# Optimization experiments

Measured on AMD Instinct MI355X. Metric: run time of the kernel, lower is better.

The kernel has to match this reference:

```python
import jax, jax.numpy as jnp
import numpy as np
import math

EMB_DIM = 1024
NUM_HEADS = 16
D_H = EMB_DIM // NUM_HEADS
B, S = 2, 2048


def setup_inputs() -> dict:
    key = jax.random.key(0)
    ks = jax.random.split(key, 6)
    limit = math.sqrt(6.0 / (EMB_DIM + D_H))  # xavier_uniform per head
    x = jax.random.normal(ks[0], (B, S, EMB_DIM), dtype=jnp.float32)
    Wq = jax.random.uniform(ks[1], (NUM_HEADS, EMB_DIM, D_H), jnp.float32, -limit, limit)
    Wk = jax.random.uniform(ks[2], (NUM_HEADS, EMB_DIM, D_H), jnp.float32, -limit, limit)
    Wv = jax.random.uniform(ks[3], (NUM_HEADS, EMB_DIM, D_H), jnp.float32, -limit, limit)
    bq = jnp.zeros((NUM_HEADS, D_H), jnp.float32)
    bk = jnp.zeros((NUM_HEADS, D_H), jnp.float32)
    bv = jnp.zeros((NUM_HEADS, D_H), jnp.float32)
    limo = math.sqrt(6.0 / (EMB_DIM + EMB_DIM))
    W_O = jax.random.uniform(ks[4], (EMB_DIM, EMB_DIM), jnp.float32, -limo, limo)
    causal_mask = jnp.tril(jnp.ones((S, S), jnp.float32))
    padding_mask = jnp.zeros((B, S), jnp.bool_)  # all-False: nothing padded
    return {"x": x, "Wq": Wq, "bq": bq, "Wk": Wk, "bk": bk, "Wv": Wv,
            "bv": bv, "W_O": W_O, "causal_mask": causal_mask,
            "padding_mask": padding_mask}


def reference(x, Wq, bq, Wk, bk, Wv, bv, W_O, causal_mask, padding_mask):
    # Per-head projections, vectorized over heads: [B,S,E] x [H,E,D] -> [B,H,S,D]
    Q = jnp.einsum('bse,hed->bhsd', x, Wq) + bq[None, :, None, :]
    K = jnp.einsum('bse,hed->bhsd', x, Wk) + bk[None, :, None, :]
    V = jnp.einsum('bse,hed->bhsd', x, Wv) + bv[None, :, None, :]
    scores = jnp.einsum('bhsd,bhtd->bhst', Q, K) / math.sqrt(D_H)
    neg_inf = jnp.float32(-jnp.inf)
    scores = jnp.where(causal_mask[None, None, :, :] == 0, neg_inf, scores)
    scores = jnp.where(padding_mask[:, None, None, :], neg_inf, scores)
    attn = jax.nn.softmax(scores, axis=-1)
    out = jnp.einsum('bhst,bhtd->bhsd', attn, V)  # [B,H,S,D]
    # concat heads in order (dim=-1) -> [B,S,H*D]
    x_concat = out.transpose(0, 2, 1, 3).reshape(B, S, EMB_DIM)
    return x_concat @ W_O
```

## Files before the change

kernel.cpp:

```cpp
#include <hip/hip_runtime.h>
#include <hip/hip_bf16.h>


typedef __hip_bfloat16 bf16;
typedef __attribute__((ext_vector_type(8))) short bfrag;
typedef __attribute__((ext_vector_type(4))) float f32x4;
typedef __attribute__((ext_vector_type(16))) float f32x16;
typedef __attribute__((ext_vector_type(4))) short short4v;

#define MFMA16(a, b, c) __builtin_amdgcn_mfma_f32_16x16x32_bf16(a, b, c, 0, 0, 0)
#define MFMA32(a, b, c) __builtin_amdgcn_mfma_f32_32x32x16_bf16(a, b, c, 0, 0, 0)

__device__ __forceinline__ unsigned pk2(float a, float b) {
  union { __hip_bfloat162 h; unsigned u; } w;
  w.h = __float22bfloat162_rn(make_float2(a, b));
  return w.u;
}

__device__ __forceinline__ void gload16(const bf16* g, bf16* l) {
  __builtin_amdgcn_global_load_lds(
      (const __attribute__((address_space(1))) void*)(g),
      (__attribute__((address_space(3))) void*)(l), 16, 0, 0);
}

__global__ __launch_bounds__(256) void prep_all(const float* __restrict__ x,
                                                const float* __restrict__ Wq,
                                                const float* __restrict__ Wk,
                                                const float* __restrict__ Wv,
                                                const float* __restrict__ Wo,
                                                bf16* __restrict__ xb,
                                                bf16* __restrict__ WqkvT,
                                                bf16* __restrict__ WoT) {
  __shared__ bf16 tile[64][80];
  int id = blockIdx.x;
  int t = threadIdx.x;
  if (id < 2048) {
    int i = id * 2048 + t * 8;
    float4 a = *(const float4*)(x + i);
    float4 b = *(const float4*)(x + i + 4);
    union { bf16 h[8]; bfrag v; } tmp;
    tmp.h[0] = __float2bfloat16(a.x); tmp.h[1] = __float2bfloat16(a.y);
    tmp.h[2] = __float2bfloat16(a.z); tmp.h[3] = __float2bfloat16(a.w);
    tmp.h[4] = __float2bfloat16(b.x); tmp.h[5] = __float2bfloat16(b.y);
    tmp.h[6] = __float2bfloat16(b.z); tmp.h[7] = __float2bfloat16(b.w);
    *(bfrag*)(xb + i) = tmp.v;
    return;
  }
  int wid = id - 2048;
  const float* src;
  bf16* dst;
  int srcld, dstld, r0, c0;
  if (wid < 768) {
    int w = wid >> 8, h = (wid >> 4) & 15;
    r0 = (wid & 15) * 64; c0 = 0;
    src = ((w == 0) ? Wq : (w == 1) ? Wk : Wv) + (long)h * 1024 * 64;
    dst = WqkvT + ((long)w * 1024 + h * 64) * 1024;
    srcld = 64; dstld = 1024;
  } else {
    int j = wid - 768;
    c0 = (j & 15) * 64; r0 = (j >> 4) * 64;
    src = Wo; dst = WoT;
    srcld = 1024; dstld = 1024;
  }
  int lr = t >> 3, lc = (t & 7) << 3;
#pragma unroll
  for (int p = 0; p < 2; ++p) {
    int r = lr + p * 32;
    const float* s = src + (long)(r0 + r) * srcld + c0 + lc;
    union { bf16 h8[8]; bfrag v; } tmp;
#pragma unroll
    for (int j = 0; j < 8; ++j) tmp.h8[j] = __float2bfloat16(s[j]);
    *(bfrag*)(&tile[r][lc]) = tmp.v;
  }
  __syncthreads();
#pragma unroll
  for (int p = 0; p < 2; ++p) {
    int c = lr + p * 32;
    union { bf16 h8[8]; bfrag v; } tmp;
#pragma unroll
    for (int j = 0; j < 8; ++j) tmp.h8[j] = tile[lc + j][c];
    *(bfrag*)(dst + (long)(c0 + c) * dstld + r0 + lc) = tmp.v;
  }
}

__global__ __launch_bounds__(256) void gemm_qkv128(const bf16* __restrict__ xb,
                                                   const bf16* __restrict__ WT,
                                                   const float* __restrict__ bq,
                                                   const float* __restrict__ bk,
                                                   const float* __restrict__ bv,
                                                   bf16* __restrict__ Q,
                                                   bf16* __restrict__ K_,
                                                   bf16* __restrict__ Vt) {
  const int K = 1024;
  __shared__ bf16 As[2][128 * 32];
  __shared__ bf16 Bs[2][128 * 32];
  int id = blockIdx.x;
  int xcd = id & 7, sw = id >> 3;
  int m0 = ((xcd << 2) | (sw & 3)) * 128;
  int n0 = (sw >> 2) * 128;
  int t = threadIdx.x, wave = t >> 6, lane = t & 63, quad = lane >> 4, col = lane & 15;
  int wr = (wave >> 1) * 64, wc = (wave & 1) * 64;
  f32x4 acc[4][4] = {};

  int schunk = (lane & 3) ^ ((lane >> 2) & 3);
  const bf16* Asrc = xb + (long)(m0 + wave * 32 + (lane >> 2)) * K + schunk * 8;
  const bf16* Bsrc = WT + (long)(n0 + wave * 32 + (lane >> 2)) * K + schunk * 8;
  int l0 = (wave * 32) * 32;
  int rdoff = ((quad ^ (col & 3)) << 3);

#define QKV_STAGE(bi, koff)                                    \
  {                                                            \
    gload16(Asrc + (koff), &As[bi][l0]);                       \
    gload16(Asrc + (koff) + 16 * K, &As[bi][l0 + 16 * 32]);    \
    gload16(Bsrc + (koff), &Bs[bi][l0]);                       \
    gload16(Bsrc + (koff) + 16 * K, &Bs[bi][l0 + 16 * 32]);    \
  }

  QKV_STAGE(0, 0);
  __syncthreads();
  for (int k0 = 0; k0 < K; k0 += 32) {
    int cur = (k0 >> 5) & 1;
    if (k0 + 32 < K) QKV_STAGE(cur ^ 1, k0 + 32);
    bfrag ra[4], rb[4];
#pragma unroll
    for (int i = 0; i < 4; ++i)
      ra[i] = *(const bfrag*)(&As[cur][(wr + 16 * i + col) * 32 + rdoff]);
#pragma unroll
    for (int c = 0; c < 4; ++c)
      rb[c] = *(const bfrag*)(&Bs[cur][(wc + 16 * c + col) * 32 + rdoff]);
#pragma unroll
    for (int c = 0; c < 4; ++c)
#pragma unroll
      for (int i = 0; i < 4; ++i) acc[c][i] = MFMA16(ra[i], rb[c], acc[c][i]);
    __syncthreads();
  }
#undef QKV_STAGE

  int sel = n0 >> 10;
  const float* bias = (sel == 0) ? bq : (sel == 1) ? bk : bv;
  float qs = (sel == 0) ? 0.18033688f : 1.0f;
#pragma unroll
  for (int c = 0; c < 4; ++c) {
    int nn = (n0 + wc + 16 * c + col) & 1023;
    float bvv = bias[nn];
    int h = nn >> 6, d = nn & 63;
#pragma unroll
    for (int i = 0; i < 4; ++i) {
      int mb = m0 + wr + 16 * i + quad * 4;
      int b = mb >> 11, s0 = mb & 2047;
      if (sel < 2) {
        bf16* dst = (sel == 0) ? Q : K_;
        long base = ((long)((b << 4) + h) * 2048 + s0) * 64 + d;
#pragma unroll
        for (int r = 0; r < 4; ++r)
          dst[base + (long)r * 64] = __float2bfloat16((acc[c][i][r] + bvv) * qs);
      } else {
        union { bf16 h4[4]; short4v v; } pk;
#pragma unroll
        for (int r = 0; r < 4; ++r) pk.h4[r] = __float2bfloat16(acc[c][i][r] + bvv);
        *(short4v*)(Vt + (long)(((b << 4) + h) * 64 + d) * 2048 + s0) = pk.v;
      }
    }
  }
}

__global__ __launch_bounds__(256) void gemm_out(const bf16* __restrict__ O,
                                                const bf16* __restrict__ Bt,
                                                float* __restrict__ Cf) {
  const int K = 1024;
  __shared__ bf16 As[2][128 * 32];
  __shared__ bf16 Bs[2][64 * 32];
  int id = blockIdx.x;
  int xcd = id & 7, sw = id >> 3;
  int m0 = ((xcd << 2) | (sw & 3)) * 128;
  int n0 = (sw >> 2) * 64;
  int t = threadIdx.x;
  int wave = t >> 6, lane = t & 63, quad = lane >> 4, col = lane & 15;
  int wr = (wave >> 1) * 64, wc = (wave & 1) * 32;
  f32x4 acc[2][4] = {};

  int schunk = (lane & 3) ^ ((lane >> 2) & 3);
  int arow = m0 + wave * 32 + (lane >> 2);
  int ob = arow >> 11, os = arow & 2047;
  const bf16* Asrc = O + (long)ob * 2097152 + (long)os * 64 + schunk * 8;
  const bf16* Bsrc = Bt + (long)(n0 + wave * 16 + (lane >> 2)) * K + schunk * 8;
  int la0 = (wave * 32) * 32;
  int lb0 = (wave * 16) * 32;
  int rdoff = ((quad ^ (col & 3)) << 3);

#define OUT_STAGE(bi, k0n)                                            \
  {                                                                   \
    long ka = ((long)((k0n) >> 6)) * 131072 + ((k0n) & 32);           \
    gload16(Asrc + ka, &As[bi][la0]);                                 \
    gload16(Asrc + ka + 16 * 64, &As[bi][la0 + 16 * 32]);             \
    gload16(Bsrc + (k0n), &Bs[bi][lb0]);                              \
  }

  OUT_STAGE(0, 0);
  __syncthreads();
  for (int k0 = 0; k0 < K; k0 += 32) {
    int cur = (k0 >> 5) & 1;
    if (k0 + 32 < K) OUT_STAGE(cur ^ 1, k0 + 32);
    bfrag ra[4], rb[2];
#pragma unroll
    for (int i = 0; i < 4; ++i)
      ra[i] = *(const bfrag*)(&As[cur][(wr + 16 * i + col) * 32 + rdoff]);
#pragma unroll
    for (int c = 0; c < 2; ++c)
      rb[c] = *(const bfrag*)(&Bs[cur][(wc + 16 * c + col) * 32 + rdoff]);
#pragma unroll
    for (int c = 0; c < 2; ++c)
#pragma unroll
      for (int i = 0; i < 4; ++i) acc[c][i] = MFMA16(ra[i], rb[c], acc[c][i]);
    __syncthreads();
  }
#undef OUT_STAGE

#pragma unroll
  for (int c = 0; c < 2; ++c) {
    int n = n0 + wc + 16 * c + col;
#pragma unroll
    for (int i = 0; i < 4; ++i)
#pragma unroll
      for (int r = 0; r < 4; ++r) {
        int m = m0 + wr + 16 * i + quad * 4 + r;
        Cf[(long)m * 1024 + n] = acc[c][i][r];
      }
  }
}

__global__ __launch_bounds__(256) void attn_kernel(const bf16* __restrict__ Q,
                                                   const bf16* __restrict__ K_,
                                                   const bf16* __restrict__ Vt,
                                                   bf16* __restrict__ O) {
  int id = blockIdx.x;
  int xcd = id & 7, jj = id >> 3;
  int qt = 31 - (jj >> 2);
  int bh = ((jj & 3) << 3) | xcd;

  __shared__ bf16 Ks[128][72];
  __shared__ bf16 Vs[64][136];

  int t = threadIdx.x, wave = t >> 6, lane = t & 63;
  int qh = wave >> 1, jh = wave & 1, hi = lane >> 5, l5 = lane & 31;

  int krow = t >> 3, kg = (t & 7) * 8;
  int vrow = t >> 4, vg = (t & 15) * 8;
  const bf16* KuBase = K_ + (long)bh * 2048 * 64;
  const bf16* VuBase = Vt + (long)bh * 64 * 2048;
  int kL = krow * 64 + kg;
  int vL = vrow * 2048 + vg;

  int q0 = qt * 64;
  int nj = (qt >> 1) + 1;
  int qi = q0 + 32 * qh + l5;

  bfrag qa[4];
  const bf16* qp = Q + ((long)bh * 2048 + q0 + 32 * qh + l5) * 64 + hi * 8;
#pragma unroll
  for (int kd = 0; kd < 4; ++kd) qa[kd] = *(const bfrag*)(qp + kd * 16);

  f32x16 o0, o1;
  float lsum = 0.f;
#pragma unroll
  for (int r = 0; r < 16; ++r) { o0[r] = 0.f; o1[r] = 0.f; }

  bfrag kreg[4], vreg[4];
#pragma unroll
  for (int i = 0; i < 4; ++i) {
    kreg[i] = *(const bfrag*)(KuBase + kL + i * 2048);
    vreg[i] = *(const bfrag*)(VuBase + vL + i * 32768);
  }

  for (int jt = 0; jt < nj; ++jt) {
    int j0 = jt * 128;
    __syncthreads();
#pragma unroll
    for (int i = 0; i < 4; ++i) {
      *(bfrag*)(&Ks[krow + 32 * i][kg]) = kreg[i];
      *(bfrag*)(&Vs[vrow + 16 * i][vg]) = vreg[i];
    }
    int jn = (jt + 1 < nj) ? j0 + 128 : j0;
    const bf16* kp = KuBase + (long)jn * 64;
    const bf16* vp = VuBase + jn;
#pragma unroll
    for (int i = 0; i < 4; ++i) {
      kreg[i] = *(const bfrag*)(kp + kL + i * 2048);
      vreg[i] = *(const bfrag*)(vp + vL + i * 32768);
    }
    __syncthreads();

    bool lastT = (jt == nj - 1);
    if (lastT && jh == 1 && ((qt & 1) == 0)) continue;

    f32x16 s0, s1;
#pragma unroll
    for (int r = 0; r < 16; ++r) { s0[r] = 0.f; s1[r] = 0.f; }
    __builtin_amdgcn_s_setprio(1);
#pragma unroll
    for (int kd = 0; kd < 4; ++kd) {
      bfrag ka0 = *(const bfrag*)(&Ks[jh * 64 + l5][kd * 16 + hi * 8]);
      bfrag ka1 = *(const bfrag*)(&Ks[jh * 64 + 32 + l5][kd * 16 + hi * 8]);
      s0 = MFMA32(ka0, qa[kd], s0);
      s1 = MFMA32(ka1, qa[kd], s1);
    }
    __builtin_amdgcn_s_setprio(0);

    unsigned g[2][4][2];
#pragma unroll
    for (int jb = 0; jb < 2; ++jb) {
      float pv[16];
      float ls = 0.f;
#pragma unroll
      for (int r = 0; r < 16; ++r) {
        int jl = (r & 3) + 8 * (r >> 2) + 4 * hi;
        int j = j0 + jh * 64 + jb * 32 + jl;
        float sv = jb ? s1[r] : s0[r];
        float p = __builtin_amdgcn_exp2f(sv);
        if (lastT) p = (j <= qi) ? p : 0.f;
        ls += p;
        pv[r] = p;
      }
      lsum += ls;
#pragma unroll
      for (int gg = 0; gg < 4; ++gg) {
        g[jb][gg][0] = pk2(pv[4 * gg], pv[4 * gg + 1]);
        g[jb][gg][1] = pk2(pv[4 * gg + 2], pv[4 * gg + 3]);
      }
    }

    __builtin_amdgcn_s_setprio(1);
#pragma unroll
    for (int jb = 0; jb < 2; ++jb) {
#pragma unroll
      for (int c = 0; c < 2; ++c) {
        unsigned a0 = g[jb][2 * c][0], a1 = g[jb][2 * c][1];
        unsigned b0 = g[jb][2 * c + 1][0], b1 = g[jb][2 * c + 1][1];
        asm("v_permlane32_swap_b32 %0, %1" : "+v"(a0), "+v"(b0));
        asm("v_permlane32_swap_b32 %0, %1" : "+v"(a1), "+v"(b1));
        union { unsigned u[4]; bfrag f; } pf;
        pf.u[0] = a0;
        pf.u[1] = a1;
        pf.u[2] = b0;
        pf.u[3] = b1;
        int kk = jh * 64 + jb * 32 + c * 16 + hi * 8;
        bfrag av0 = *(const bfrag*)(&Vs[l5][kk]);
        bfrag av1 = *(const bfrag*)(&Vs[32 + l5][kk]);
        o0 = MFMA32(av0, pf.f, o0);
        o1 = MFMA32(av1, pf.f, o1);
      }
    }
    __builtin_amdgcn_s_setprio(0);
  }

  lsum += __shfl_xor(lsum, 32, 64);

  __syncthreads();
  float* Osc = (float*)&Ks[0][0];
  float* Lsc = (float*)&Vs[0][0];
  bf16* Of = (bf16*)((char*)&Vs[0][0] + 512);
  int q = 32 * qh + l5;
  if (jh == 1) {
#pragma unroll
    for (int r = 0; r < 16; ++r) {
      int d = (r & 3) + 8 * (r >> 2) + 4 * hi;
      Osc[q * 68 + d] = o0[r];
      Osc[q * 68 + 32 + d] = o1[r];
    }
    if (hi == 0) Lsc[q] = lsum;
  }
  __syncthreads();
  if (jh == 0) {
    float inv = 1.f / (lsum + Lsc[q]);
#pragma unroll
    for (int r = 0; r < 16; ++r) {
      int d = (r & 3) + 8 * (r >> 2) + 4 * hi;
      Of[q * 72 + d] = __float2bfloat16((o0[r] + Osc[q * 68 + d]) * inv);
      Of[q * 72 + 32 + d] = __float2bfloat16((o1[r] + Osc[q * 68 + 32 + d]) * inv);
    }
  }
  __syncthreads();
  int row = t >> 2, off = (t & 3) * 16;
  bf16* po = O + ((long)bh * 2048 + q0 + row) * 64 + off;
  *(bfrag*)(po) = *(const bfrag*)(&Of[row * 72 + off]);
  *(bfrag*)(po + 8) = *(const bfrag*)(&Of[row * 72 + off + 8]);
}

extern "C" void kernel_launch(void* const* d_in, const int* in_sizes, int n_in,
                              void* d_out, int out_size, void* d_ws, size_t ws_size,
                              hipStream_t stream) {
  const float* x  = (const float*)d_in[0];
  const float* Wq = (const float*)d_in[1];
  const float* bq = (const float*)d_in[2];
  const float* Wk = (const float*)d_in[3];
  const float* bk = (const float*)d_in[4];
  const float* Wv = (const float*)d_in[5];
  const float* bv = (const float*)d_in[6];
  const float* Wo = (const float*)d_in[7];
  float* out = (float*)d_out;

  bf16* ws = (bf16*)d_ws;
  const long MB1 = 1 << 20;
  bf16* WqkvT = ws + 0 * MB1;
  bf16* WoT   = ws + 3 * MB1;
  bf16* Q     = ws + 4 * MB1;
  bf16* K_    = ws + 8 * MB1;
  bf16* Vt    = ws + 12 * MB1;
  bf16* O     = ws + 16 * MB1;
  bf16* xb    = ws + 20 * MB1;

  prep_all<<<3072, 256, 0, stream>>>(x, Wq, Wk, Wv, Wo, xb, WqkvT, WoT);
  gemm_qkv128<<<768, 256, 0, stream>>>(xb, WqkvT, bq, bk, bv, Q, K_, Vt);
  attn_kernel<<<1024, 256, 0, stream>>>(Q, K_, Vt, O);
  gemm_out<<<512, 256, 0, stream>>>(O, WoT, out);
}
```

Baseline: 194.8 us.

## Rewrite QKV GEMM as 256x256 tile, 8-wave kernel with phased prefetch pipeline

Replaces the 128x128 QKV projection GEMM with a 256x256-tile kernel using 512 threads, 128 KB of dynamic LDS with 64-wide K chunks, and an 8-phase software pipeline. Each phase interleaves LDS fragment reads, async global-to-LDS loads for later stages, raw barriers, and MFMA bursts under raised wave priority. The larger tile raises data reuse per byte loaded and the pipelining hides load latency. The cost is a grid of only 192 blocks and higher register and LDS pressure per block, which may hurt occupancy.

New measurement: 192.1 us. Within noise of the previous version (-1.4%).

```diff
diff --git a/kernel.cpp b/kernel.cpp
--- a/kernel.cpp
+++ b/kernel.cpp
@@ -21,6 +21,12 @@
   __builtin_amdgcn_global_load_lds(
       (const __attribute__((address_space(1))) void*)(g),
       (__attribute__((address_space(3))) void*)(l), 16, 0, 0);
+}
+
+__device__ __forceinline__ void barrier_raw() {
+  asm volatile("" ::: "memory");
+  __builtin_amdgcn_s_barrier();
+  asm volatile("" ::: "memory");
 }
 
 __global__ __launch_bounds__(256) void prep_all(const float* __restrict__ x,
@@ -83,82 +89,113 @@
   }
 }
 
-__global__ __launch_bounds__(256) void gemm_qkv128(const bf16* __restrict__ xb,
-                                                   const bf16* __restrict__ WT,
-                                                   const float* __restrict__ bq,
-                                                   const float* __restrict__ bk,
-                                                   const float* __restrict__ bv,
-                                                   bf16* __restrict__ Q,
-                                                   bf16* __restrict__ K_,
-                                                   bf16* __restrict__ Vt) {
-  const int K = 1024;
-  __shared__ bf16 As[2][128 * 32];
-  __shared__ bf16 Bs[2][128 * 32];
+__global__ __launch_bounds__(512, 2) void gemm_qkv128(const bf16* __restrict__ xb,
+                                                      const bf16* __restrict__ WT,
+                                                      const float* __restrict__ bq,
+                                                      const float* __restrict__ bk,
+                                                      const float* __restrict__ bv,
+                                                      bf16* __restrict__ Q,
+                                                      bf16* __restrict__ K_,
+                                                      bf16* __restrict__ Vt) {
+  extern __shared__ bf16 lds[];
   int id = blockIdx.x;
-  int xcd = id & 7, sw = id >> 3;
-  int m0 = ((xcd << 2) | (sw & 3)) * 128;
-  int n0 = (sw >> 2) * 128;
-  int t = threadIdx.x, wave = t >> 6, lane = t & 63, quad = lane >> 4, col = lane & 15;
-  int wr = (wave >> 1) * 64, wc = (wave & 1) * 64;
-  f32x4 acc[4][4] = {};
-
-  int schunk = (lane & 3) ^ ((lane >> 2) & 3);
-  const bf16* Asrc = xb + (long)(m0 + wave * 32 + (lane >> 2)) * K + schunk * 8;
-  const bf16* Bsrc = WT + (long)(n0 + wave * 32 + (lane >> 2)) * K + schunk * 8;
-  int l0 = (wave * 32) * 32;
-  int rdoff = ((quad ^ (col & 3)) << 3);
-
-#define QKV_STAGE(bi, koff)                                    \
-  {                                                            \
-    gload16(Asrc + (koff), &As[bi][l0]);                       \
-    gload16(Asrc + (koff) + 16 * K, &As[bi][l0 + 16 * 32]);    \
-    gload16(Bsrc + (koff), &Bs[bi][l0]);                       \
-    gload16(Bsrc + (koff) + 16 * K, &Bs[bi][l0 + 16 * 32]);    \
-  }
-
-  QKV_STAGE(0, 0);
-  __syncthreads();
-  for (int k0 = 0; k0 < K; k0 += 32) {
-    int cur = (k0 >> 5) & 1;
-    if (k0 + 32 < K) QKV_STAGE(cur ^ 1, k0 + 32);
-    bfrag ra[4], rb[4];
-#pragma unroll
-    for (int i = 0; i < 4; ++i)
-      ra[i] = *(const bfrag*)(&As[cur][(wr + 16 * i + col) * 32 + rdoff]);
-#pragma unroll
-    for (int c = 0; c < 4; ++c)
-      rb[c] = *(const bfrag*)(&Bs[cur][(wc + 16 * c + col) * 32 + rdoff]);
-#pragma unroll
-    for (int c = 0; c < 4; ++c)
-#pragma unroll
-      for (int i = 0; i < 4; ++i) acc[c][i] = MFMA16(ra[i], rb[c], acc[c][i]);
-    __syncthreads();
-  }
-#undef QKV_STAGE
+  int xcd = id & 7, idx = id >> 3;
+  int tile = xcd * 24 + idx;
+  int mt = tile & 15, nt = tile >> 4;
+  int m0 = mt * 256, n0 = nt * 256;
+
+  int t = threadIdx.x;
+  int wave = t >> 6, lane = t & 63, quad = lane >> 4, col = lane & 15;
+  int wm = wave >> 2, wn = wave & 3;
+
+  int schunk = 8 * ((t & 7) ^ ((t >> 3) & 7));
+  const bf16* aSrc = xb + (long)(m0 + (t >> 3)) * 1024 + schunk;
+  const bf16* bSrc = WT + (long)(n0 + (t >> 3)) * 1024 + schunk;
+  int wv512 = wave * 512;
+
+  int xoff0 = (quad * 8) ^ ((col & 7) << 3);
+  const bf16* aRdB = lds + wm * 8192 + col * 64;
+  const bf16* bRdB = lds + 32768 + (wn >> 1) * 8192 + (wn & 1) * 4096 + col * 64;
+
+  f32x4 acc[8][4] = {};
+
+#define STA(BUF, HALF, G, KS)                                                  \
+  gload16(aSrc + (long)((HALF)*128 + (G)*64) * 1024 + (KS)*64,                 \
+          lds + (BUF)*16384 + (HALF)*8192 + (G)*4096 + wv512)
+#define STB(BUF, HALF, G, KS)                                                  \
+  gload16(bSrc + (long)((HALF)*128 + (G)*64) * 1024 + (KS)*64,                 \
+          lds + 32768 + (BUF)*16384 + (HALF)*8192 + (G)*4096 + wv512)
+
+#define PHASE(BUF, MH, KC, STAGES, VMW)                                        \
+  {                                                                            \
+    int xk = xoff0 ^ ((KC)*32);                                                \
+    bfrag ra[4], rb[4];                                                        \
+    _Pragma("unroll") for (int u = 0; u < 4; ++u) {                            \
+      ra[u] = *(const bfrag*)(aRdB + (BUF)*16384 + (MH)*4096 + u * 1024 + xk); \
+      rb[u] = *(const bfrag*)(bRdB + (BUF)*16384 + u * 1024 + xk);             \
+    }                                                                          \
+    STAGES;                                                                    \
+    VMW;                                                                       \
+    barrier_raw();                                                             \
+    __builtin_amdgcn_s_setprio(1);                                             \
+    _Pragma("unroll") for (int ni = 0; ni < 4; ++ni)                           \
+      _Pragma("unroll") for (int mi2 = 0; mi2 < 4; ++mi2)                      \
+        acc[(MH)*4 + mi2][ni] = MFMA16(ra[mi2], rb[ni], acc[(MH)*4 + mi2][ni]);\
+    __builtin_amdgcn_s_setprio(0);                                             \
+    barrier_raw();                                                             \
+  }
+
+#define VM2 asm volatile("s_waitcnt vmcnt(2)" ::: "memory")
+#define NOVM
+
+  STA(0, 0, 0, 0); STA(0, 1, 0, 0); STA(0, 0, 1, 0); STA(0, 1, 1, 0);
+  STB(0, 0, 0, 0); STB(0, 0, 1, 0); STB(0, 1, 0, 0); STB(0, 1, 1, 0);
+  STA(1, 0, 0, 1); STA(1, 1, 0, 1);
+  VM2;
+  barrier_raw();
+
+  for (int it = 0; it < 8; ++it) {
+    int ksB = 2 * it + 1;
+    int kA  = (it < 7) ? 2 * it + 2 : 14;
+    int ksB2 = (it < 7) ? 2 * it + 3 : 15;
+    PHASE(0, 0, 0, { STA(1, 0, 1, ksB); STA(1, 1, 1, ksB); }, NOVM);
+    PHASE(0, 0, 1, { STB(1, 0, 0, ksB); STB(1, 0, 1, ksB); }, NOVM);
+    PHASE(0, 1, 0, { STB(1, 1, 0, ksB); STB(1, 1, 1, ksB); }, NOVM);
+    PHASE(0, 1, 1, { STA(0, 0, 0, kA); STA(0, 1, 0, kA); }, VM2);
+    PHASE(1, 0, 0, { STA(0, 0, 1, kA); STA(0, 1, 1, kA); }, NOVM);
+    PHASE(1, 0, 1, { STB(0, 0, 0, kA); STB(0, 0, 1, kA); }, NOVM);
+    PHASE(1, 1, 0, { STB(0, 1, 0, kA); STB(0, 1, 1, kA); }, NOVM);
+    PHASE(1, 1, 1, { STA(1, 0, 0, ksB2); STA(1, 1, 0, ksB2); }, VM2);
+  }
+#undef PHASE
+#undef STA
+#undef STB
+#undef VM2
+#undef NOVM
 
   int sel = n0 >> 10;
   const float* bias = (sel == 0) ? bq : (sel == 1) ? bk : bv;
   float qs = (sel == 0) ? 0.18033688f : 1.0f;
 #pragma unroll
-  for (int c = 0; c < 4; ++c) {
-    int nn = (n0 + wc + 16 * c + col) & 1023;
+  for (int ni = 0; ni < 4; ++ni) {
+    int nn = (n0 + wn * 64 + ni * 16 + col) & 1023;
     float bvv = bias[nn];
     int h = nn >> 6, d = nn & 63;
 #pragma unroll
-    for (int i = 0; i < 4; ++i) {
-      int mb = m0 + wr + 16 * i + quad * 4;
-      int b = mb >> 11, s0 = mb & 2047;
+    for (int mi = 0; mi < 8; ++mi) {
+      int mb = m0 + wm * 128 + mi * 16 + quad * 4;
+      int b = mb >> 11, s0q = mb & 2047;
       if (sel < 2) {
         bf16* dst = (sel == 0) ? Q : K_;
-        long base = ((long)((b << 4) + h) * 2048 + s0) * 64 + d;
+        long base = ((long)((b << 4) + h) * 2048 + s0q) * 64 + d;
 #pragma unroll
         for (int r = 0; r < 4; ++r)
-          dst[base + (long)r * 64] = __float2bfloat16((acc[c][i][r] + bvv) * qs);
+          dst[base + (long)r * 64] = __float2bfloat16((acc[mi][ni][r] + bvv) * qs);
       } else {
         union { bf16 h4[4]; short4v v; } pk;
 #pragma unroll
-        for (int r = 0; r < 4; ++r) pk.h4[r] = __float2bfloat16(acc[c][i][r] + bvv);
-        *(short4v*)(Vt + (long)(((b << 4) + h) * 64 + d) * 2048 + s0) = pk.v;
+        for (int r = 0; r < 4; ++r) pk.h4[r] = __float2bfloat16(acc[mi][ni][r] + bvv);
+        *(short4v*)(Vt + (long)(((b << 4) + h) * 64 + d) * 2048 + s0q) = pk.v;
       }
     }
   }
@@ -410,7 +447,7 @@
   bf16* xb    = ws + 20 * MB1;
 
   prep_all<<<3072, 256, 0, stream>>>(x, Wq, Wk, Wv, Wo, xb, WqkvT, WoT);
-  gemm_qkv128<<<768, 256, 0, stream>>>(xb, WqkvT, bq, bk, bv, Q, K_, Vt);
+  gemm_qkv128<<<192, 512, 131072, stream>>>(xb, WqkvT, bq, bk, bv, Q, K_, Vt);
   attn_kernel<<<1024, 256, 0, stream>>>(Q, K_, Vt, O);
   gemm_out<<<512, 256, 0, stream>>>(O, WoT, out);
 }
```
